# Kernel optimization log

Hardware: AMD Instinct MI355X
Metric: run time of the kernel (lower is better)

Reference implementation:

```python
import jax, jax.numpy as jnp
import numpy as np

B, N = 8, 4096  # batch of epidemic trajectories, nodes in the contact network


def setup_inputs() -> dict:
    key = jax.random.key(0)
    k1, k2, k3, k4 = jax.random.split(key, 4)
    state = jax.random.uniform(k1, (B, 4, N), dtype=jnp.float32)
    state = state / state.sum(axis=1, keepdims=True)  # per-node SEIR distribution
    ISNet = jax.random.uniform(k2, (N, N), dtype=jnp.float32)  # dense contact weights in [0,1)
    # small transition probs so rows sum < 1 (expand_psMatrix stays a valid stochastic matrix)
    psMatrix = jax.random.uniform(k3, (4, 4), dtype=jnp.float32) * 0.05
    U = jax.random.uniform(k4, (N,), dtype=jnp.float32)  # torch.rand(n) draw, shared across batch
    return {"state": state, "ISNet": ISNet, "psMatrix": psMatrix, "U": U}


def _expand_ps(psMatrix):
    # eye * (1 - row_sum) + psMatrix  (adds the stay-in-state probability)
    stable = 1.0 - psMatrix.sum(axis=1)
    return jnp.eye(4, dtype=psMatrix.dtype) * stable + psMatrix


def _step(state, ISNet, psMatrix):
    psM = _expand_ps(psMatrix)
    p01 = psM[0, 1]
    # lp[b,j,k] = log(1 - ISNet[j,k] * S_b[j] * I_b[k] * p01)   (vectorized over batch)
    lp = jnp.log(1.0 - ISNet[None, :, :] * state[:, 0, :, None] * state[:, 2, None, :] * p01)
    ps1 = 1.0 - jnp.exp(lp.sum(axis=2))  # [B, N] infection probability per node
    zeros = jnp.zeros_like(ps1)
    ps10 = jnp.stack([1.0 - ps1, ps1, zeros, zeros], axis=1)  # [B, 4, N]
    # constantM zeroes the S row of psM before the transpose-matmul
    mask = jnp.array([[0.0, 0, 0, 0], [1, 1, 1, 1], [1, 1, 1, 1], [1, 1, 1, 1]], dtype=psM.dtype)
    ps2T = (psM * mask).T  # [4, 4]
    return state[:, 0][:, None, :] * ps10 + jnp.einsum('ij,bjn->bin', ps2T, state)


def _sample(P, U):
    # cumulative-threshold sampling: first compartment whose running sum crosses U fires
    u = jnp.broadcast_to(U[None, :], P[:, 0, :].shape)  # [B, N], shared draw across batch
    outs = []
    for i in range(P.shape[1]):  # fixed 4 compartments
        u = u - P[:, i, :]
        s = (u < 0).astype(P.dtype)
        outs.append(s)
        u = u + s
    return jnp.stack(outs, axis=1)  # [B, 4, N] one-hot per node


def reference(state, ISNet, psMatrix, U):
    new_state = _step(state, ISNet, psMatrix)
    return _sample(new_state, U)
```

## Files before the change

kernel.cpp:

```cpp
#include <hip/hip_runtime.h>

#define NN 4096
#define BB 8
#define JT 4


__device__ __forceinline__ float2 pk_mul(float2 a, float2 b) {
    return make_float2(a.x * b.x, a.y * b.y);
}
__device__ __forceinline__ float2 pk_add(float2 a, float2 b) {
    return make_float2(a.x + b.x, a.y + b.y);
}
__device__ __forceinline__ float2 pk_fnma(float2 a, float2 b, float2 c) {
    return make_float2(fmaf(-a.x, b.x, c.x), fmaf(-a.y, b.y, c.y));
}

__global__ __launch_bounds__(256, 4) void epi_kernel(
    const float* __restrict__ state,
    const float* __restrict__ ISNet,
    const float* __restrict__ psMatrix,
    const float* __restrict__ U,
    float* __restrict__ out)
{
    const int j0   = blockIdx.x * JT;
    const int tid  = threadIdx.x;
    const int wave = tid >> 6;
    const int lane = tid & 63;
    const int b0   = wave * 2;

    const float p01 = psMatrix[1];

    float  cf[JT][2];
    double prod[JT][2];
    #pragma unroll
    for (int jj = 0; jj < JT; ++jj) {
        #pragma unroll
        for (int bi = 0; bi < 2; ++bi) {
            cf[jj][bi]   = state[(size_t)(b0 + bi) * 4 * NN + (j0 + jj)] * p01;
            prod[jj][bi] = 1.0;
        }
    }

    const float4* __restrict__ w0 = (const float4*)(ISNet + (size_t)(j0 + 0) * NN);
    const float4* __restrict__ w1 = (const float4*)(ISNet + (size_t)(j0 + 1) * NN);
    const float4* __restrict__ w2 = (const float4*)(ISNet + (size_t)(j0 + 2) * NN);
    const float4* __restrict__ w3 = (const float4*)(ISNet + (size_t)(j0 + 3) * NN);
    const float4* __restrict__ i0 = (const float4*)(state + ((size_t)(b0 + 0) * 4 + 2) * NN);
    const float4* __restrict__ i1 = (const float4*)(state + ((size_t)(b0 + 1) * 4 + 2) * NN);

    float4 wA[JT], wB[JT], wC[JT], ia[2], ib[2];

#define LW(BUF, IDX)                                        \
    do {                                                    \
        const int _x = lane + (IDX) * 64;                   \
        BUF[0] = w0[_x]; BUF[1] = w1[_x];                   \
        BUF[2] = w2[_x]; BUF[3] = w3[_x];                   \
    } while (0)
#define LI(BUF, IDX)                                        \
    do {                                                    \
        const int _x = lane + (IDX) * 64;                   \
        BUF[0] = i0[_x]; BUF[1] = i1[_x];                   \
    } while (0)

    auto compute = [&](const float4 (&W)[JT], const float4 (&I)[2]) {
        #pragma unroll
        for (int jj = 0; jj < JT; ++jj) {
            const float2 w01 = make_float2(W[jj].x, W[jj].y);
            const float2 w23 = make_float2(W[jj].z, W[jj].w);
            #pragma unroll
            for (int bi = 0; bi < 2; ++bi) {
                const float2 c2  = make_float2(cf[jj][bi], cf[jj][bi]);
                const float2 i01 = make_float2(I[bi].x, I[bi].y);
                const float2 i23 = make_float2(I[bi].z, I[bi].w);
                const float2 z01 = pk_mul(pk_mul(c2, w01), i01);
                const float2 z23 = pk_mul(pk_mul(c2, w23), i23);
                const float2 q2  = pk_fnma(z01, z23, pk_add(z01, z23));
                const float  q   = fmaf(-q2.x, q2.y, q2.x + q2.y);
                prod[jj][bi] = fma(-(double)q, prod[jj][bi], prod[jj][bi]);
            }
        }
    };

#define STEP(W, I, K)                                       \
    do {                                                    \
        compute(W, I);                                      \
        if ((K) + 3 < 16) LW(W, (K) + 3);                   \
        if ((K) + 2 < 16) LI(I, (K) + 2);                   \
    } while (0)

    LW(wA, 0); LI(ia, 0); LW(wB, 1); LI(ib, 1); LW(wC, 2);

    STEP(wA, ia, 0);  STEP(wB, ib, 1);  STEP(wC, ia, 2);  STEP(wA, ib, 3);
    STEP(wB, ia, 4);  STEP(wC, ib, 5);  STEP(wA, ia, 6);  STEP(wB, ib, 7);
    STEP(wC, ia, 8);  STEP(wA, ib, 9);  STEP(wB, ia, 10); STEP(wC, ib, 11);
    STEP(wA, ia, 12); STEP(wB, ib, 13); STEP(wC, ia, 14); STEP(wA, ib, 15);
#undef STEP
#undef LW
#undef LI

    #pragma unroll
    for (int off = 32; off >= 8; off >>= 1) {
        #pragma unroll
        for (int jj = 0; jj < JT; ++jj) {
            #pragma unroll
            for (int bi = 0; bi < 2; ++bi)
                prod[jj][bi] *= __shfl_xor(prod[jj][bi], off, 64);
        }
    }

    const int g = lane >> 3;
    double v = prod[0][0];
    v = (g == 1) ? prod[0][1] : v;
    v = (g == 2) ? prod[1][0] : v;
    v = (g == 3) ? prod[1][1] : v;
    v = (g == 4) ? prod[2][0] : v;
    v = (g == 5) ? prod[2][1] : v;
    v = (g == 6) ? prod[3][0] : v;
    v = (g == 7) ? prod[3][1] : v;
    v *= __shfl_down(v, 4, 64);
    v *= __shfl_down(v, 2, 64);
    v *= __shfl_down(v, 1, 64);

    __shared__ double red[JT][BB];
    if ((lane & 7) == 0)
        red[g >> 1][b0 + (g & 1)] = v;
    __syncthreads();

    if (tid < JT * BB) {
        const int jj = tid >> 3, b = tid & 7;
        const int j  = j0 + jj;
        const double tot = red[jj][b];
        const double ps1 = 1.0 - tot;

        double pm[4][4];
        #pragma unroll
        for (int r = 0; r < 4; ++r) {
            double s = 0.0;
            #pragma unroll
            for (int q = 0; q < 4; ++q) {
                pm[r][q] = (double)psMatrix[r * 4 + q];
                s += pm[r][q];
            }
            pm[r][r] += (1.0 - s);
        }

        double st[4];
        #pragma unroll
        for (int r = 0; r < 4; ++r)
            st[r] = (double)state[(size_t)b * 4 * NN + r * NN + j];

        const double S = st[0];
        const double ps10[4] = {1.0 - ps1, ps1, 0.0, 0.0};

        double P[4];
        #pragma unroll
        for (int i = 0; i < 4; ++i) {
            double acc = S * ps10[i];
            #pragma unroll
            for (int r = 1; r < 4; ++r)
                acc += pm[r][i] * st[r];
            P[i] = acc;
        }

        double u = (double)U[j];
        #pragma unroll
        for (int i = 0; i < 4; ++i) {
            u -= P[i];
            const double s = (u < 0.0) ? 1.0 : 0.0;
            out[(size_t)b * 4 * NN + i * NN + j] = (float)s;
            u += s;
        }
    }
}

extern "C" void kernel_launch(void* const* d_in, const int* in_sizes, int n_in,
                              void* d_out, int out_size, void* d_ws, size_t ws_size,
                              hipStream_t stream) {
    const float* state    = (const float*)d_in[0];
    const float* ISNet    = (const float*)d_in[1];
    const float* psMatrix = (const float*)d_in[2];
    const float* U        = (const float*)d_in[3];
    float* out            = (float*)d_out;

    epi_kernel<<<NN / JT, 256, 0, stream>>>(state, ISNet, psMatrix, U, out);
}
```

Before: 23.98 us.

## Stage ISNet rows through double-buffered LDS shared across waves

Each wave now loads one ISNet row in 1024-column chunks into a double-buffered shared-memory tile, and all four waves read the four rows from LDS. Before, every wave loaded all four rows from global memory. The change cuts redundant global/L2 traffic for ISNet by a factor of four. In exchange it adds 32KB of LDS per block, which may reduce occupancy, plus per-chunk __syncthreads barriers and LDS read traffic.

Result: slower. 34.19 us (+42.6%).

```diff
diff --git a/kernel.cpp b/kernel.cpp
--- a/kernel.cpp
+++ b/kernel.cpp
@@ -3,6 +3,8 @@
 #define NN 4096
 #define BB 8
 #define JT 4
+#define CK 1024
+#define NC (NN / CK)
 
 
 __device__ __forceinline__ float2 pk_mul(float2 a, float2 b) {
@@ -28,6 +30,9 @@
     const int lane = tid & 63;
     const int b0   = wave * 2;
 
+    __shared__ float  wlds[2][JT][CK];
+    __shared__ double red[JT][BB];
+
     const float p01 = psMatrix[1];
 
     float  cf[JT][2];
@@ -41,37 +46,36 @@
         }
     }
 
-    const float4* __restrict__ w0 = (const float4*)(ISNet + (size_t)(j0 + 0) * NN);
-    const float4* __restrict__ w1 = (const float4*)(ISNet + (size_t)(j0 + 1) * NN);
-    const float4* __restrict__ w2 = (const float4*)(ISNet + (size_t)(j0 + 2) * NN);
-    const float4* __restrict__ w3 = (const float4*)(ISNet + (size_t)(j0 + 3) * NN);
-    const float4* __restrict__ i0 = (const float4*)(state + ((size_t)(b0 + 0) * 4 + 2) * NN);
-    const float4* __restrict__ i1 = (const float4*)(state + ((size_t)(b0 + 1) * 4 + 2) * NN);
-
-    float4 wA[JT], wB[JT], wC[JT], ia[2], ib[2];
-
-#define LW(BUF, IDX)                                        \
-    do {                                                    \
-        const int _x = lane + (IDX) * 64;                   \
-        BUF[0] = w0[_x]; BUF[1] = w1[_x];                   \
-        BUF[2] = w2[_x]; BUF[3] = w3[_x];                   \
+    const float* __restrict__ wrow = ISNet + (size_t)(j0 + wave) * NN;
+    const float4* __restrict__ i0  = (const float4*)(state + ((size_t)(b0 + 0) * 4 + 2) * NN);
+    const float4* __restrict__ i1  = (const float4*)(state + ((size_t)(b0 + 1) * 4 + 2) * NN);
+
+    float4 stg[4];
+
+#define LOAD_STAGE(C)                                               \
+    do {                                                            \
+        const float4* _src = (const float4*)(wrow + (C) * CK);      \
+        _Pragma("unroll")                                           \
+        for (int g = 0; g < 4; ++g) stg[g] = _src[g * 64 + lane];   \
     } while (0)
-#define LI(BUF, IDX)                                        \
-    do {                                                    \
-        const int _x = lane + (IDX) * 64;                   \
-        BUF[0] = i0[_x]; BUF[1] = i1[_x];                   \
+#define WRITE_STAGE(BUF)                                            \
+    do {                                                            \
+        _Pragma("unroll")                                           \
+        for (int g = 0; g < 4; ++g)                                 \
+            *((float4*)&wlds[BUF][wave][(g * 64 + lane) * 4]) = stg[g]; \
     } while (0)
 
-    auto compute = [&](const float4 (&W)[JT], const float4 (&I)[2]) {
+    auto compute = [&](const float4 (&W)[JT], const float4& I0, const float4& I1) {
         #pragma unroll
         for (int jj = 0; jj < JT; ++jj) {
             const float2 w01 = make_float2(W[jj].x, W[jj].y);
             const float2 w23 = make_float2(W[jj].z, W[jj].w);
             #pragma unroll
             for (int bi = 0; bi < 2; ++bi) {
+                const float4& I  = bi ? I1 : I0;
                 const float2 c2  = make_float2(cf[jj][bi], cf[jj][bi]);
-                const float2 i01 = make_float2(I[bi].x, I[bi].y);
-                const float2 i23 = make_float2(I[bi].z, I[bi].w);
+                const float2 i01 = make_float2(I.x, I.y);
+                const float2 i23 = make_float2(I.z, I.w);
                 const float2 z01 = pk_mul(pk_mul(c2, w01), i01);
                 const float2 z23 = pk_mul(pk_mul(c2, w23), i23);
                 const float2 q2  = pk_fnma(z01, z23, pk_add(z01, z23));
@@ -81,22 +85,34 @@
         }
     };
 
-#define STEP(W, I, K)                                       \
-    do {                                                    \
-        compute(W, I);                                      \
-        if ((K) + 3 < 16) LW(W, (K) + 3);                   \
-        if ((K) + 2 < 16) LI(I, (K) + 2);                   \
-    } while (0)
-
-    LW(wA, 0); LI(ia, 0); LW(wB, 1); LI(ib, 1); LW(wC, 2);
-
-    STEP(wA, ia, 0);  STEP(wB, ib, 1);  STEP(wC, ia, 2);  STEP(wA, ib, 3);
-    STEP(wB, ia, 4);  STEP(wC, ib, 5);  STEP(wA, ia, 6);  STEP(wB, ib, 7);
-    STEP(wC, ia, 8);  STEP(wA, ib, 9);  STEP(wB, ia, 10); STEP(wC, ib, 11);
-    STEP(wA, ia, 12); STEP(wB, ib, 13); STEP(wC, ia, 14); STEP(wA, ib, 15);
-#undef STEP
-#undef LW
-#undef LI
+    LOAD_STAGE(0);
+    WRITE_STAGE(0);
+    LOAD_STAGE(1);
+
+    for (int c = 0; c < NC; ++c) {
+        __syncthreads();
+        if (c + 1 < NC) WRITE_STAGE((c + 1) & 1);
+        if (c + 2 < NC) LOAD_STAGE(c + 2);
+
+        float4 iv0[4], iv1[4];
+        #pragma unroll
+        for (int g = 0; g < 4; ++g) {
+            const int x = (c * CK / 4) + g * 64 + lane;
+            iv0[g] = i0[x];
+            iv1[g] = i1[x];
+        }
+
+        #pragma unroll
+        for (int it = 0; it < 4; ++it) {
+            float4 wv[JT];
+            #pragma unroll
+            for (int jj = 0; jj < JT; ++jj)
+                wv[jj] = *((const float4*)&wlds[c & 1][jj][(it * 64 + lane) * 4]);
+            compute(wv, iv0[it], iv1[it]);
+        }
+    }
+#undef LOAD_STAGE
+#undef WRITE_STAGE
 
     #pragma unroll
     for (int off = 32; off >= 8; off >>= 1) {
@@ -121,7 +137,6 @@
     v *= __shfl_down(v, 2, 64);
     v *= __shfl_down(v, 1, 64);
 
-    __shared__ double red[JT][BB];
     if ((lane & 7) == 0)
         red[g >> 1][b0 + (g & 1)] = v;
     __syncthreads();
```
